# Optimization experiments

Measured on AMD Instinct MI355X. Metric: run time of the kernel, lower is better.

## Reference

```python
import jax, jax.numpy as jnp
import numpy as np


def setup_inputs() -> dict:
    key = jax.random.key(0)
    k1, k2, k3, k4 = jax.random.split(key, 4)
    B, CIN, H, W = 4, 64, 512, 512
    COUT, K, WDIM = 64, 3, 512
    x = jax.random.normal(k1, (B, CIN, H, W), jnp.float32)
    w = jax.random.normal(k2, (B, WDIM), jnp.float32)
    # init_std = 1/lrmul = 1.0 for both weights (lrmul=1)
    conv_w = jax.random.normal(k3, (K, K, CIN, COUT), jnp.float32)
    mod_w = jax.random.normal(k4, (WDIM, CIN), jnp.float32)
    mod_b = jnp.zeros((CIN,), jnp.float32)
    return {"x": x, "w": w, "conv_w": conv_w, "mod_w": mod_w, "mod_b": mod_b}


def reference(x, w, conv_w, mod_w, mod_b):
    B, Cin, H, W_ = x.shape
    K, _, _, Cout = conv_w.shape
    wdim = mod_w.shape[0]
    # Dense (gain=1, lrmul=1): runtime_coef = 1/sqrt(fan_in)
    rc_dense = np.float32(1.0 / np.sqrt(wdim))
    # BiasAct linear (lrmul=1, gain=1): just add bias; then +1.0
    style = w @ (rc_dense * mod_w) + mod_b + 1.0  # [B, Cin]
    # conv weight runtime coef (gain=1, lrmul=1)
    rc_conv = np.float32(1.0 / np.sqrt(K * K * Cin))
    # per-sample modulated weight [B, K, K, Cin, Cout]
    wt = (rc_conv * conv_w)[None] * style[:, None, None, :, None]
    # demodulate over (kh, kw, Cin)
    d = jax.lax.rsqrt(jnp.sum(wt * wt, axis=(1, 2, 3)) + 1e-8)  # [B, Cout]
    wt = wt * d[:, None, None, None, :]
    # transpose to [K, K, Cin, B, Cout] and fold batch into output channels
    wt = jnp.transpose(wt, (1, 2, 3, 0, 4)).reshape(K, K, Cin, B * Cout)
    # grouped conv: groups = B
    xg = x.reshape(1, B * Cin, H, W_)
    out = jax.lax.conv_general_dilated(
        xg, wt,
        window_strides=(1, 1),
        padding="SAME",
        dimension_numbers=("NCHW", "HWIO", "NCHW"),
        feature_group_count=B,
    )
    return out.reshape(B, Cout, H, W_)
```

## Files before the change

### kernel.cpp

```cpp
#include <hip/hip_runtime.h>


typedef __bf16 bf16x8 __attribute__((ext_vector_type(8)));
typedef float f32x4 __attribute__((ext_vector_type(4)));
typedef unsigned short ushortx8 __attribute__((ext_vector_type(8)));

#define CIN   64
#define COUT  64
#define HH    512
#define WW    512
#define WDIM  512

#define TILE_H 8
#define TILE_W 32
#define XR     10
#define XC     34
#define CPAD   72

__device__ __forceinline__ unsigned short f2bf(float f) {
    unsigned int u = __float_as_uint(f);
    unsigned int r = (u + 0x7FFFu + ((u >> 16) & 1u)) >> 16;
    return (unsigned short)r;
}

__global__ void prep_kernel(const float* __restrict__ wv,
                            const float* __restrict__ conv_w,
                            const float* __restrict__ mod_w,
                            const float* __restrict__ mod_b,
                            unsigned short* __restrict__ Wswz) {
    const int b    = blockIdx.x;
    const int tid  = threadIdx.x;
    const int lane6 = tid & 63;
    const int part  = tid >> 6;
    __shared__ float red[256];
    __shared__ float style[64];
    __shared__ float dsc[64];
    const float rc_dense = 0.04419417382415922f;
    const float rc_conv  = 0.041666666666666664f;

    float s = 0.f;
    const float* wb = wv + b * WDIM;
    for (int k = part * 128; k < part * 128 + 128; ++k)
        s += wb[k] * mod_w[k * 64 + lane6];
    red[tid] = s;
    __syncthreads();
    if (part == 0) {
        float tot = red[lane6] + red[64 + lane6] + red[128 + lane6] + red[192 + lane6];
        style[lane6] = tot * rc_dense + mod_b[lane6] + 1.0f;
    }
    __syncthreads();

    float qq = 0.f;
    for (int idx = part * 144; idx < part * 144 + 144; ++idx) {
        float v = conv_w[idx * 64 + lane6] * style[idx & 63];
        qq += v * v;
    }
    red[tid] = qq;
    __syncthreads();
    if (part == 0) {
        float tot = red[lane6] + red[64 + lane6] + red[128 + lane6] + red[192 + lane6];
        dsc[lane6] = rsqrtf(rc_conv * rc_conv * tot + 1e-8f);
    }
    __syncthreads();

    for (int it = 0; it < 18; ++it) {
        int id  = it * 256 + tid;
        int l   = id & 63;
        int mf  = (id >> 6) & 3;
        int ks  = (id >> 8) & 1;
        int t   = id >> 9;
        int co  = mf * 16 + (l & 15);
        int ci0 = ks * 32 + (l >> 4) * 8;
        float fco = rc_conv * dsc[co];
        ushortx8 ov;
#pragma unroll
        for (int j = 0; j < 8; ++j) {
            int ci = ci0 + j;
            float v = conv_w[(t * 64 + ci) * 64 + co] * style[ci] * fco;
            ov[j] = f2bf(v);
        }
        *reinterpret_cast<ushortx8*>(Wswz + (size_t)b * 36864 + id * 8) = ov;
    }
}

__global__ __launch_bounds__(256, 3) void conv_kernel(
        const float* __restrict__ x,
        const unsigned short* __restrict__ Wswz,
        float* __restrict__ out) {
    __shared__ unsigned short xs[XR * XC * CPAD];

    const int tid  = threadIdx.x;
    const int blk  = blockIdx.x;
    const int b    = blk >> 10;
    const int tile = blk & 1023;
    const int tr   = tile >> 4;
    const int tc   = tile & 15;
    const int h0   = tr * TILE_H;
    const int w0   = tc * TILE_W;
    const float* xb = x + (size_t)b * CIN * HH * WW;

    for (int it = 0; it < 11; ++it) {
        int id = it * 256 + tid;
        if (id < 2720) {
            int c   = id % 34;
            int rem = id / 34;
            int r   = rem % 10;
            int o8  = rem / 10;
            int rg  = h0 + r - 1;
            int cg  = w0 + c - 1;
            ushortx8 v;
            if (((unsigned)rg < (unsigned)HH) && ((unsigned)cg < (unsigned)WW)) {
                const float* p = xb + ((size_t)(o8 * 8) * HH + rg) * WW + cg;
#pragma unroll
                for (int j = 0; j < 8; ++j)
                    v[j] = f2bf(p[(size_t)j * HH * WW]);
            } else {
#pragma unroll
                for (int j = 0; j < 8; ++j) v[j] = 0;
            }
            *reinterpret_cast<ushortx8*>(&xs[(r * XC + c) * CPAD + o8 * 8]) = v;
        }
    }
    __syncthreads();

    const int l   = tid & 63;
    const int wv  = tid >> 6;
    const int m16 = l & 15;
    const int q   = l >> 4;

    f32x4 acc[4][4];
#pragma unroll
    for (int mf = 0; mf < 4; ++mf)
#pragma unroll
        for (int nf = 0; nf < 4; ++nf)
            acc[mf][nf] = (f32x4){0.f, 0.f, 0.f, 0.f};

    int Xbase[4];
#pragma unroll
    for (int nf = 0; nf < 4; ++nf) {
        int np = (wv * 4 + nf) * 16 + m16;
        int pr = np >> 5, pc = np & 31;
        Xbase[nf] = (pr * XC + pc) * CPAD + q * 8;
    }
    const unsigned short* Wb = Wswz + (size_t)b * 36864 + l * 8;

    for (int kh = 0; kh < 3; ++kh) {
        for (int kw = 0; kw < 3; ++kw) {
            int t = kh * 3 + kw;
#pragma unroll
            for (int s = 0; s < 2; ++s) {
                const unsigned short* Wt = Wb + (t * 2 + s) * 2048;
                bf16x8 a[4], bb[4];
#pragma unroll
                for (int mf = 0; mf < 4; ++mf)
                    a[mf] = *reinterpret_cast<const bf16x8*>(Wt + mf * 512);
                int so = (kh * XC + kw) * CPAD + s * 32;
#pragma unroll
                for (int nf = 0; nf < 4; ++nf)
                    bb[nf] = *reinterpret_cast<const bf16x8*>(&xs[Xbase[nf] + so]);
#pragma unroll
                for (int mf = 0; mf < 4; ++mf)
#pragma unroll
                    for (int nf = 0; nf < 4; ++nf)
                        acc[mf][nf] = __builtin_amdgcn_mfma_f32_16x16x32_bf16(
                            a[mf], bb[nf], acc[mf][nf], 0, 0, 0);
            }
        }
    }

    float* ob = out + (size_t)b * COUT * HH * WW;
#pragma unroll
    for (int nf = 0; nf < 4; ++nf) {
        int np = (wv * 4 + nf) * 16 + m16;
        int pr = np >> 5, pc = np & 31;
        int h = h0 + pr, wc = w0 + pc;
#pragma unroll
        for (int mf = 0; mf < 4; ++mf) {
            int co = mf * 16 + q * 4;
            float* po = ob + ((size_t)co * HH + h) * WW + wc;
#pragma unroll
            for (int reg = 0; reg < 4; ++reg)
                po[(size_t)reg * HH * WW] = acc[mf][nf][reg];
        }
    }
}

extern "C" void kernel_launch(void* const* d_in, const int* in_sizes, int n_in,
                              void* d_out, int out_size, void* d_ws, size_t ws_size,
                              hipStream_t stream) {
    const float* x      = (const float*)d_in[0];
    const float* w      = (const float*)d_in[1];
    const float* conv_w = (const float*)d_in[2];
    const float* mod_w  = (const float*)d_in[3];
    const float* mod_b  = (const float*)d_in[4];
    float* out = (float*)d_out;
    unsigned short* Wswz = (unsigned short*)d_ws;

    prep_kernel<<<4, 256, 0, stream>>>(w, conv_w, mod_w, mod_b, Wswz);
    conv_kernel<<<4096, 256, 0, stream>>>(x, Wswz, out);
}
```

Baseline: 547.4 us.

## Pre-convert input to padded NHWC bf16 and stage tiles via direct global-to-LDS loads

Adds a pass that converts the fp32 NCHW input once into a zero-padded NHWC bf16 buffer in workspace, plus a kernel that zeroes its border ring. The conv kernel then loads halo tiles with direct global-to-LDS 16-byte loads using an XOR swizzle instead of per-thread strided fp32 gathers and converts, and writes output with nontemporal stores. This removes the redundant strided reads and halo re-conversion across tiles. In exchange it adds an extra full read/write pass over the input and needs a large workspace, falling back to the old kernel otherwise.

```diff
diff --git a/kernel.cpp b/kernel.cpp
--- a/kernel.cpp
+++ b/kernel.cpp
@@ -16,6 +16,11 @@
 #define XR     10
 #define XC     34
 #define CPAD   72
+
+#define PW        514
+#define XP_BATCH  (514 * 514 * 64)
+#define WSWZ_USH  147456
+#define NEED_WS   (294912ull + 4ull * 514 * 514 * 64 * 2)
 
 __device__ __forceinline__ unsigned short f2bf(float f) {
     unsigned int u = __float_as_uint(f);
@@ -83,6 +88,142 @@
     }
 }
 
+__global__ void ring_kernel(unsigned short* __restrict__ Xp) {
+    int id = blockIdx.x * 256 + threadIdx.x;
+    if (id >= 65664) return;
+    int b  = id / 16416;
+    int r  = id - b * 16416;
+    int px = r >> 3, ck = r & 7;
+    int rp, cp;
+    if (px < 514)       { rp = 0;             cp = px; }
+    else if (px < 1028) { rp = 513;           cp = px - 514; }
+    else if (px < 1540) { rp = px - 1028 + 1; cp = 0; }
+    else                { rp = px - 1540 + 1; cp = 513; }
+    ushortx8 z = {0, 0, 0, 0, 0, 0, 0, 0};
+    *reinterpret_cast<ushortx8*>(
+        Xp + (size_t)b * XP_BATCH + ((size_t)rp * PW + cp) * 64 + ck * 8) = z;
+}
+
+__global__ __launch_bounds__(256) void convert_kernel(const float* __restrict__ x,
+                                                      unsigned short* __restrict__ Xp) {
+    const int tid = threadIdx.x;
+    const int blk = blockIdx.x;
+#pragma unroll
+    for (int it = 0; it < 4; ++it) {
+        unsigned id = (unsigned)blk * 1024u + (unsigned)(it * 256 + tid);
+        int ck = id & 7;
+        int w  = (id >> 3) & 511;
+        int h  = (id >> 12) & 511;
+        int b  = id >> 21;
+        const float* xp = x + ((size_t)(b * 64 + ck * 8) * (HH * WW) + (size_t)h * WW + w);
+        ushortx8 v;
+#pragma unroll
+        for (int j = 0; j < 8; ++j)
+            v[j] = f2bf(__builtin_nontemporal_load(xp + (size_t)j * (HH * WW)));
+        *reinterpret_cast<ushortx8*>(
+            Xp + (size_t)b * XP_BATCH + ((size_t)(h + 1) * PW + (w + 1)) * 64 + ck * 8) = v;
+    }
+}
+
+__global__ __launch_bounds__(256, 3) void conv2_kernel(
+        const unsigned short* __restrict__ Xp,
+        const unsigned short* __restrict__ Wswz,
+        float* __restrict__ out) {
+    __shared__ alignas(16) unsigned short xs[XR * XC * 64];
+
+    const int tid  = threadIdx.x;
+    const int blk  = blockIdx.x;
+    const int b    = blk >> 10;
+    const int tile = blk & 1023;
+    const int tr   = tile >> 4;
+    const int tc   = tile & 15;
+    const int h0   = tr * TILE_H;
+    const int w0   = tc * TILE_W;
+    const unsigned short* Xpb = Xp + (size_t)b * XP_BATCH;
+    const int wv = tid >> 6, l = tid & 63;
+
+    for (int it = 0; it < 11; ++it) {
+        unsigned id = (unsigned)(it * 256 + tid);
+        if (id < 2720u) {
+            unsigned row = id / 272u;
+            unsigned rc  = id - row * 272u;
+            unsigned pc  = rc >> 3;
+            unsigned ck  = rc & 7u;
+            unsigned g   = ck ^ (pc & 7u);
+            const unsigned short* gp =
+                Xpb + ((size_t)(h0 + (int)row) * PW + (w0 + (int)pc)) * 64 + g * 8;
+            unsigned short* lp = xs + (size_t)(it * 256 + wv * 64) * 8;
+            __builtin_amdgcn_global_load_lds(
+                (const __attribute__((address_space(1))) void*)gp,
+                (__attribute__((address_space(3))) void*)lp, 16, 0, 0);
+        }
+    }
+    __syncthreads();
+
+    const int m16 = l & 15;
+    const int q   = l >> 4;
+
+    f32x4 acc[4][4];
+#pragma unroll
+    for (int mf = 0; mf < 4; ++mf)
+#pragma unroll
+        for (int nf = 0; nf < 4; ++nf)
+            acc[mf][nf] = (f32x4){0.f, 0.f, 0.f, 0.f};
+
+    int pix0[4], pc0[4];
+#pragma unroll
+    for (int nf = 0; nf < 4; ++nf) {
+        int np = (wv * 4 + nf) * 16 + m16;
+        int pr = np >> 5, pc = np & 31;
+        pix0[nf] = pr * XC + pc;
+        pc0[nf]  = pc;
+    }
+    const unsigned short* Wb = Wswz + (size_t)b * 36864 + l * 8;
+
+#pragma unroll
+    for (int kh = 0; kh < 3; ++kh)
+#pragma unroll
+        for (int kw = 0; kw < 3; ++kw) {
+            const int t = kh * 3 + kw;
+#pragma unroll
+            for (int s = 0; s < 2; ++s) {
+                const unsigned short* Wt = Wb + (t * 2 + s) * 2048;
+                bf16x8 a[4], bb[4];
+#pragma unroll
+                for (int mf = 0; mf < 4; ++mf)
+                    a[mf] = *reinterpret_cast<const bf16x8*>(Wt + mf * 512);
+#pragma unroll
+                for (int nf = 0; nf < 4; ++nf) {
+                    int pix = pix0[nf] + kh * XC + kw;
+                    int ck  = (s * 4 + q) ^ ((pc0[nf] + kw) & 7);
+                    bb[nf] = *reinterpret_cast<const bf16x8*>(&xs[pix * 64 + ck * 8]);
+                }
+#pragma unroll
+                for (int mf = 0; mf < 4; ++mf)
+#pragma unroll
+                    for (int nf = 0; nf < 4; ++nf)
+                        acc[mf][nf] = __builtin_amdgcn_mfma_f32_16x16x32_bf16(
+                            a[mf], bb[nf], acc[mf][nf], 0, 0, 0);
+            }
+        }
+
+    float* ob = out + (size_t)b * COUT * HH * WW;
+#pragma unroll
+    for (int nf = 0; nf < 4; ++nf) {
+        int np = (wv * 4 + nf) * 16 + m16;
+        int pr = np >> 5, pc = np & 31;
+        int h = h0 + pr, wc = w0 + pc;
+#pragma unroll
+        for (int mf = 0; mf < 4; ++mf) {
+            int co = mf * 16 + q * 4;
+            float* po = ob + ((size_t)co * HH + h) * WW + wc;
+#pragma unroll
+            for (int reg = 0; reg < 4; ++reg)
+                __builtin_nontemporal_store(acc[mf][nf][reg], po + (size_t)reg * HH * WW);
+        }
+    }
+}
+
 __global__ __launch_bounds__(256, 3) void conv_kernel(
         const float* __restrict__ x,
         const unsigned short* __restrict__ Wswz,
@@ -197,5 +338,13 @@
     unsigned short* Wswz = (unsigned short*)d_ws;
 
     prep_kernel<<<4, 256, 0, stream>>>(w, conv_w, mod_w, mod_b, Wswz);
-    conv_kernel<<<4096, 256, 0, stream>>>(x, Wswz, out);
-}
+
+    if (ws_size >= NEED_WS) {
+        unsigned short* Xp = Wswz + WSWZ_USH;
+        ring_kernel<<<257, 256, 0, stream>>>(Xp);
+        convert_kernel<<<8192, 256, 0, stream>>>(x, Xp);
+        conv2_kernel<<<4096, 256, 0, stream>>>(Xp, Wswz, out);
+    } else {
+        conv_kernel<<<4096, 256, 0, stream>>>(x, Wswz, out);
+    }
+}
```

New measurement: 585.4 us. 6.9% more time.
